# Performance work log

Hardware: AMD Instinct MI355X
Metric: run time of the kernel (lower is better)

The kernel has to match this reference:

```python
import jax, jax.numpy as jnp
import numpy as np

N_GAUSS, H, W, SH_DEG = 1024, 256, 256, 3

SH_C0 = 0.28209479177387814
SH_C1 = 0.4886025119029199
SH_C2 = (1.0925484305920792, -1.0925484305920792, 0.31539156525252005,
         -1.0925484305920792, 0.5462742152960396)
SH_C3 = (-0.5900435899266435, 2.890611442640554, -0.4570457994644658,
         0.3731763325901154, -0.4570457994644658, 1.445305721320277,
         -0.5900435899266435)


def eval_sh(shs, dirs):
    # shs: [N,16,3], dirs: [N,3] normalized. Matches computeColorFromSH (deg 3).
    x, y, z = dirs[:, 0:1], dirs[:, 1:2], dirs[:, 2:3]
    res = SH_C0 * shs[:, 0]
    res = res - SH_C1 * y * shs[:, 1] + SH_C1 * z * shs[:, 2] - SH_C1 * x * shs[:, 3]
    xx, yy, zz = x * x, y * y, z * z
    xy, yz, xz = x * y, y * z, x * z
    res = (res + SH_C2[0] * xy * shs[:, 4] + SH_C2[1] * yz * shs[:, 5]
           + SH_C2[2] * (2.0 * zz - xx - yy) * shs[:, 6]
           + SH_C2[3] * xz * shs[:, 7] + SH_C2[4] * (xx - yy) * shs[:, 8])
    res = (res + SH_C3[0] * y * (3.0 * xx - yy) * shs[:, 9]
           + SH_C3[1] * xy * z * shs[:, 10]
           + SH_C3[2] * y * (4.0 * zz - xx - yy) * shs[:, 11]
           + SH_C3[3] * z * (2.0 * zz - 3.0 * xx - 3.0 * yy) * shs[:, 12]
           + SH_C3[4] * x * (4.0 * zz - xx - yy) * shs[:, 13]
           + SH_C3[5] * z * (xx - yy) * shs[:, 14]
           + SH_C3[6] * x * (xx - yy - zz) * shs[:, 15])
    return jnp.maximum(res + 0.5, 0.0)


def render(background, means3D, opacities, scales, rotations, shs,
           view_mat, proj_mat, cam_pos, tan_fovx, tan_fovy, height, width):
    N = means3D.shape[0]
    tanx, tany = tan_fovx[0], tan_fovy[0]
    fx = width / (2.0 * tanx)
    fy = height / (2.0 * tany)

    # --- 3D covariance: Sigma = R diag(s^2) R^T (computeCov3D) ---
    q = rotations / jnp.linalg.norm(rotations, axis=-1, keepdims=True)
    r, x, y, z = q[:, 0], q[:, 1], q[:, 2], q[:, 3]
    R = jnp.stack([
        jnp.stack([1 - 2 * (y * y + z * z), 2 * (x * y - r * z), 2 * (x * z + r * y)], -1),
        jnp.stack([2 * (x * y + r * z), 1 - 2 * (x * x + z * z), 2 * (y * z - r * x)], -1),
        jnp.stack([2 * (x * z - r * y), 2 * (y * z + r * x), 1 - 2 * (x * x + y * y)], -1),
    ], -2)  # [N,3,3]
    M = R * scales[:, None, :]
    Sigma = jnp.einsum('nij,nkj->nik', M, M)  # [N,3,3]

    # --- view transform + EWA 2D covariance (computeCov2D) ---
    t = means3D @ view_mat[:3, :3].T + view_mat[:3, 3]  # [N,3] camera space
    tz = t[:, 2]
    valid_z = tz > 0.2
    tzs = jnp.where(valid_z, tz, 1.0)
    limx, limy = 1.3 * tanx, 1.3 * tany
    tx = jnp.clip(t[:, 0] / tzs, -limx, limx) * tzs
    ty = jnp.clip(t[:, 1] / tzs, -limy, limy) * tzs
    zeros = jnp.zeros_like(tzs)
    J = jnp.stack([
        jnp.stack([fx / tzs, zeros, -fx * tx / (tzs * tzs)], -1),
        jnp.stack([zeros, fy / tzs, -fy * ty / (tzs * tzs)], -1),
    ], -2)  # [N,2,3]
    T2 = jnp.einsum('nij,jk->nik', J, view_mat[:3, :3])
    cov2d = jnp.einsum('nij,njk,nlk->nil', T2, Sigma, T2)  # [N,2,2]
    a = cov2d[:, 0, 0] + 0.3
    c = cov2d[:, 1, 1] + 0.3
    b = cov2d[:, 0, 1]
    det = a * c - b * b
    valid = valid_z & (det > 0)
    inv_det = jnp.where(det > 0, 1.0 / jnp.where(det > 0, det, 1.0), 0.0)
    conic = jnp.stack([c, -b, a], -1) * inv_det[:, None]  # [N,3]

    # --- projection to pixel coords (ndc2Pix) ---
    ph = jnp.concatenate([means3D, jnp.ones((N, 1), means3D.dtype)], -1) @ proj_mat.T
    p_w = 1.0 / (ph[:, 3] + 1e-7)
    px = ((ph[:, 0] * p_w + 1.0) * width - 1.0) * 0.5
    py = ((ph[:, 1] * p_w + 1.0) * height - 1.0) * 0.5

    # --- SH -> RGB ---
    dirs = means3D - cam_pos[None, :]
    dirs = dirs / jnp.linalg.norm(dirs, axis=-1, keepdims=True)
    colors = eval_sh(shs, dirs)  # [N,3]

    # --- global depth sort (front to back) ---
    depth = jnp.where(valid, tz, 1e10)
    order = jnp.argsort(depth)
    px_s, py_s = px[order], py[order]
    conic_s = conic[order]
    opac_s = opacities[order, 0]
    colors_s = colors[order]
    valid_s = valid[order]

    # --- per-pixel alpha and front-to-back compositing (renderCUDA) ---
    ys, xs = jnp.meshgrid(jnp.arange(height, dtype=jnp.float32),
                          jnp.arange(width, dtype=jnp.float32), indexing='ij')
    pixx, pixy = xs.reshape(-1), ys.reshape(-1)  # [P]
    dx = px_s[:, None] - pixx[None, :]  # [N,P]
    dy = py_s[:, None] - pixy[None, :]
    power = (-0.5 * (conic_s[:, 0:1] * dx * dx + conic_s[:, 2:3] * dy * dy)
             - conic_s[:, 1:2] * dx * dy)
    alpha = jnp.minimum(opac_s[:, None] * jnp.exp(jnp.minimum(power, 0.0)), 0.99)
    keep = (power <= 0.0) & (alpha >= 1.0 / 255.0) & valid_s[:, None]
    alpha = jnp.where(keep, alpha, 0.0)

    Tcum = jnp.cumprod(1.0 - alpha, axis=0)  # [N,P]
    T_prev = jnp.concatenate([jnp.ones((1, alpha.shape[1]), alpha.dtype), Tcum[:-1]], 0)
    wgt = alpha * T_prev
    img = jnp.einsum('nc,np->cp', colors_s, wgt) + background[:, None] * Tcum[-1][None, :]
    return img.reshape(3, height, width)


def setup_inputs() -> dict:
    key = jax.random.key(0)
    ks = jax.random.split(key, 6)
    means3D = jax.random.uniform(ks[0], (N_GAUSS, 3), minval=-3.0, maxval=3.0)
    means3D = means3D.at[:, 2].set(
        jax.random.uniform(ks[1], (N_GAUSS,), minval=2.0, maxval=10.0))
    opacities = jax.random.uniform(ks[2], (N_GAUSS, 1), minval=0.3, maxval=0.95)
    scales = jax.random.uniform(ks[3], (N_GAUSS, 3), minval=0.02, maxval=0.15)
    rotations = jax.random.normal(ks[4], (N_GAUSS, 4))
    shs = jax.random.normal(ks[5], (N_GAUSS, (SH_DEG + 1) ** 2, 3)) * 0.3
    background = jnp.zeros((3,), jnp.float32)
    view_mat = jnp.eye(4, dtype=jnp.float32)  # camera at origin looking +z
    tanx = tany = 0.5
    zn, zf = 0.01, 100.0
    proj = np.zeros((4, 4), np.float32)
    proj[0, 0] = 1.0 / tanx
    proj[1, 1] = 1.0 / tany
    proj[2, 2] = zf / (zf - zn)
    proj[2, 3] = -(zf * zn) / (zf - zn)
    proj[3, 2] = 1.0
    proj_mat = jnp.asarray(proj) @ view_mat  # full projection
    cam_pos = jnp.zeros((3,), jnp.float32)
    return dict(background=background, means3D=means3D, opacities=opacities,
                scales=scales, rotations=rotations, shs=shs, view_mat=view_mat,
                proj_mat=proj_mat, cam_pos=cam_pos,
                tan_fovx=jnp.array([tanx], jnp.float32),
                tan_fovy=jnp.array([tany], jnp.float32), height=H, width=W)


def reference(background, means3D, opacities, scales, rotations, shs,
              view_mat, proj_mat, cam_pos, tan_fovx, tan_fovy, height, width):
    return render(background, means3D, opacities, scales, rotations, shs,
                  view_mat, proj_mat, cam_pos, tan_fovx, tan_fovy, height, width)
```

## Files before the change

### kernel.cpp

```cpp
#include <hip/hip_runtime.h>
#include <math.h>

#define NG 1024
#define LOG2E 1.4426950408889634f


__global__ void prep_kernel(
    const float* __restrict__ means3D, const float* __restrict__ opacities,
    const float* __restrict__ scales,  const float* __restrict__ rotations,
    const float* __restrict__ shs,     const float* __restrict__ view_mat,
    const float* __restrict__ proj_mat,const float* __restrict__ cam_pos,
    const float* __restrict__ tanx_p,  const float* __restrict__ tany_p,
    const int* __restrict__ h_p,       const int* __restrict__ w_p,
    uint4* __restrict__ grec, float4* __restrict__ rec, int N)
{
    int i = blockIdx.x * blockDim.x + threadIdx.x;
    if (i >= N) return;
    float tanx = tanx_p[0], tany = tany_p[0];
    float Wf = (float)w_p[0], Hf = (float)h_p[0];
    int tilesX = w_p[0] >> 3, tilesY = h_p[0] >> 3;
    float fx = Wf / (2.f * tanx), fy = Hf / (2.f * tany);

    float mx = means3D[3*i], my = means3D[3*i+1], mz = means3D[3*i+2];

    float4 q4 = ((const float4*)rotations)[i];
    float qr = q4.x, qx = q4.y, qy = q4.z, qz = q4.w;
    float qn = sqrtf(qr*qr + qx*qx + qy*qy + qz*qz);
    qr /= qn; qx /= qn; qy /= qn; qz /= qn;
    float sx = scales[3*i], sy = scales[3*i+1], sz = scales[3*i+2];
    float R00 = 1.f-2.f*(qy*qy+qz*qz), R01 = 2.f*(qx*qy-qr*qz), R02 = 2.f*(qx*qz+qr*qy);
    float R10 = 2.f*(qx*qy+qr*qz), R11 = 1.f-2.f*(qx*qx+qz*qz), R12 = 2.f*(qy*qz-qr*qx);
    float R20 = 2.f*(qx*qz-qr*qy), R21 = 2.f*(qy*qz+qr*qx), R22 = 1.f-2.f*(qx*qx+qy*qy);
    float M00=R00*sx, M01=R01*sy, M02=R02*sz;
    float M10=R10*sx, M11=R11*sy, M12=R12*sz;
    float M20=R20*sx, M21=R21*sy, M22=R22*sz;
    float S00 = M00*M00+M01*M01+M02*M02;
    float S01 = M00*M10+M01*M11+M02*M12;
    float S02 = M00*M20+M01*M21+M02*M22;
    float S11 = M10*M10+M11*M11+M12*M12;
    float S12 = M10*M20+M11*M21+M12*M22;
    float S22 = M20*M20+M21*M21+M22*M22;

    const float* V = view_mat;
    float t0 = V[0]*mx + V[1]*my + V[2]*mz  + V[3];
    float t1 = V[4]*mx + V[5]*my + V[6]*mz  + V[7];
    float t2 = V[8]*mx + V[9]*my + V[10]*mz + V[11];
    bool valid_z = t2 > 0.2f;
    float tzs = valid_z ? t2 : 1.0f;
    float limx = 1.3f*tanx, limy = 1.3f*tany;
    float txc = fminf(fmaxf(t0/tzs, -limx), limx) * tzs;
    float tyc = fminf(fmaxf(t1/tzs, -limy), limy) * tzs;
    float inv_tz = 1.f / tzs;
    float J00 = fx*inv_tz, J02 = -fx*txc*inv_tz*inv_tz;
    float J11 = fy*inv_tz, J12 = -fy*tyc*inv_tz*inv_tz;
    float T200 = J00*V[0] + J02*V[8];
    float T201 = J00*V[1] + J02*V[9];
    float T202 = J00*V[2] + J02*V[10];
    float T210 = J11*V[4] + J12*V[8];
    float T211 = J11*V[5] + J12*V[9];
    float T212 = J11*V[6] + J12*V[10];
    float u0 = S00*T200 + S01*T201 + S02*T202;
    float u1 = S01*T200 + S11*T201 + S12*T202;
    float u2 = S02*T200 + S12*T201 + S22*T202;
    float cov00 = T200*u0 + T201*u1 + T202*u2;
    float cov01 = T210*u0 + T211*u1 + T212*u2;
    float v0 = S00*T210 + S01*T211 + S02*T212;
    float v1 = S01*T210 + S11*T211 + S12*T212;
    float v2 = S02*T210 + S12*T211 + S22*T212;
    float cov11 = T210*v0 + T211*v1 + T212*v2;
    float a = cov00 + 0.3f;
    float c = cov11 + 0.3f;
    float b = cov01;
    float det = a*c - b*b;
    bool valid = valid_z && (det > 0.f);
    float inv_det = (det > 0.f) ? (1.f/det) : 0.f;
    float Aq = c*inv_det, Bq = -b*inv_det, Cq = a*inv_det;

    const float* P = proj_mat;
    float ph0 = P[0]*mx  + P[1]*my  + P[2]*mz  + P[3];
    float ph1 = P[4]*mx  + P[5]*my  + P[6]*mz  + P[7];
    float ph3 = P[12]*mx + P[13]*my + P[14]*mz + P[15];
    float pw = 1.f / (ph3 + 1e-7f);
    float px = ((ph0*pw + 1.f)*Wf - 1.f)*0.5f;
    float py = ((ph1*pw + 1.f)*Hf - 1.f)*0.5f;

    float dxm = mx - cam_pos[0], dym = my - cam_pos[1], dzm = mz - cam_pos[2];
    float dn = sqrtf(dxm*dxm + dym*dym + dzm*dzm);
    float X = dxm/dn, Y = dym/dn, Z = dzm/dn;
    float xx = X*X, yy = Y*Y, zz = Z*Z;
    float xy = X*Y, yz = Y*Z, xz = X*Z;
    float sc[48];
    {
        const float4* s4 = (const float4*)(shs + i*48);
        #pragma unroll
        for (int k = 0; k < 12; k++) {
            float4 v = s4[k];
            sc[4*k] = v.x; sc[4*k+1] = v.y; sc[4*k+2] = v.z; sc[4*k+3] = v.w;
        }
    }
    float col[3];
    #pragma unroll
    for (int ch = 0; ch < 3; ch++) {
        float res = 0.28209479177387814f * sc[ch];
        res += -0.4886025119029199f * Y * sc[3+ch]
             +  0.4886025119029199f * Z * sc[6+ch]
             -  0.4886025119029199f * X * sc[9+ch];
        res +=  1.0925484305920792f * xy * sc[12+ch]
             + (-1.0925484305920792f) * yz * sc[15+ch]
             +  0.31539156525252005f * (2.f*zz - xx - yy) * sc[18+ch]
             + (-1.0925484305920792f) * xz * sc[21+ch]
             +  0.5462742152960396f * (xx - yy) * sc[24+ch];
        res += -0.5900435899266435f * Y * (3.f*xx - yy) * sc[27+ch]
             +  2.890611442640554f  * xy * Z * sc[30+ch]
             + (-0.4570457994644658f) * Y * (4.f*zz - xx - yy) * sc[33+ch]
             +  0.3731763325901154f  * Z * (2.f*zz - 3.f*xx - 3.f*yy) * sc[36+ch]
             + (-0.4570457994644658f) * X * (4.f*zz - xx - yy) * sc[39+ch]
             +  1.445305721320277f   * Z * (xx - yy) * sc[42+ch]
             + (-0.5900435899266435f) * X * (xx - yy - zz) * sc[45+ch];
        col[ch] = fmaxf(res + 0.5f, 0.f);
    }

    float op = valid ? opacities[i] : 0.f;
    float dpt = valid ? t2 : 1e10f;

    float tau = 2.f * logf(255.f * fmaxf(op, 1e-20f));
    bool has = valid && (op * 255.f > 1.f) && (tau > 0.f);
    float rx = has ? (sqrtf(tau * a) + 0.01f) : 0.f;
    float ry = has ? (sqrtf(tau * c) + 0.01f) : 0.f;

    unsigned trange = 255u;
    if (has) {
        int tx0 = (int)ceilf((px - rx - 7.f) * 0.125f);
        int tx1 = (int)floorf((px + rx) * 0.125f);
        int ty0 = (int)ceilf((py - ry - 7.f) * 0.125f);
        int ty1 = (int)floorf((py + ry) * 0.125f);
        tx0 = max(tx0, 0); ty0 = max(ty0, 0);
        tx1 = min(tx1, tilesX - 1); ty1 = min(ty1, tilesY - 1);
        if (tx0 <= tx1 && ty0 <= ty1)
            trange = (unsigned)tx0 | ((unsigned)tx1 << 8)
                   | ((unsigned)ty0 << 16) | ((unsigned)ty1 << 24);
    }
    grec[i] = make_uint4(__float_as_uint(dpt), (unsigned)i, trange, 0u);

    rec[i*3 + 0] = make_float4(px, py, -0.5f*LOG2E*Aq, -LOG2E*Bq);
    rec[i*3 + 1] = make_float4(-0.5f*LOG2E*Cq, op, col[0], col[1]);
    rec[i*3 + 2] = make_float4(col[2], 0.f, 0.f, 0.f);
}

__device__ inline unsigned long long bstage_shfl(unsigned long long key,
                                                 int tid, int j, int k) {
    unsigned long long partner = __shfl_xor(key, j, 64);
    bool lower = (tid & j) == 0;
    bool asc   = (tid & k) == 0;
    return ((key < partner) == (lower == asc)) ? key : partner;
}

__device__ inline float rlane(float v, int l) {
    return __int_as_float(__builtin_amdgcn_readlane(__float_as_int(v), l));
}

__global__ void __launch_bounds__(64) render_kernel(
    const uint4* __restrict__ grec,
    const float4* __restrict__ rec,
    const float* __restrict__ background,
    float* __restrict__ out,
    int N, int W, int HW)
{
    __shared__ unsigned long long skey[NG];
    int tile = blockIdx.x;
    int tilesX = W >> 3;
    int tx = tile % tilesX, ty = tile / tilesX;
    int lane = threadIdx.x;
    int lx = lane & 7, ly = lane >> 3;
    float pixx = (float)(tx*8 + lx);
    float pixy = (float)(ty*8 + ly);

    int cnt = 0;
    const uint4 miss = make_uint4(0u, 0u, 255u, 0u);
    for (int base = 0; base < N; base += 256) {
        int g0 = base + lane;
        uint4 ra = (g0       < N) ? grec[g0]       : miss;
        uint4 rb = (g0 + 64  < N) ? grec[g0 + 64]  : miss;
        uint4 rc = (g0 + 128 < N) ? grec[g0 + 128] : miss;
        uint4 rd = (g0 + 192 < N) ? grec[g0 + 192] : miss;
        #pragma unroll
        for (int s = 0; s < 4; s++) {
            uint4 r = (s == 0) ? ra : (s == 1) ? rb : (s == 2) ? rc : rd;
            unsigned tr = r.z;
            bool hit = (tx >= (int)(tr & 255u)) & (tx <= (int)((tr >> 8) & 255u))
                     & (ty >= (int)((tr >> 16) & 255u)) & (ty <= (int)(tr >> 24));
            unsigned long long mask = __ballot(hit);
            if (hit) {
                int pos = cnt + __popcll(mask & ((1ull << lane) - 1ull));
                skey[pos] = ((unsigned long long)r.x << 32) | r.y;
            }
            cnt += __popcll(mask);
        }
    }
    __syncthreads();

    float T = 1.f, Cr = 0.f, Cg = 0.f, Cb = 0.f;
    if (cnt > 0 && cnt <= 64) {
        unsigned long long key = (lane < cnt) ? skey[lane] : ~0ull;
        for (int k = 2; k <= 64; k <<= 1)
            for (int j = k >> 1; j >= 1; j >>= 1)
                key = bstage_shfl(key, lane, j, k);
        int gg = (lane < cnt) ? (int)(unsigned)key : 0;
        float4 r0 = rec[gg*3 + 0];
        float4 r1 = rec[gg*3 + 1];
        float4 r2 = rec[gg*3 + 2];
        for (int m = 0; m < cnt; m++) {
            float gpx = rlane(r0.x, m), gpy = rlane(r0.y, m);
            float gA  = rlane(r0.z, m), gB  = rlane(r0.w, m);
            float gC  = rlane(r1.x, m), gop = rlane(r1.y, m);
            float gcr = rlane(r1.z, m), gcg = rlane(r1.w, m);
            float gcb = rlane(r2.x, m);
            float dx = gpx - pixx, dy = gpy - pixy;
            float p2 = fmaf(gA, dx*dx, fmaf(gC, dy*dy, gB*(dx*dy)));
            float e  = __builtin_amdgcn_exp2f(p2);
            float alpha = fminf(gop * e, 0.99f);
            float a2 = (alpha >= (1.f/255.f)) ? alpha : 0.f;
            float w = a2 * T;
            Cr = fmaf(gcr, w, Cr);
            Cg = fmaf(gcg, w, Cg);
            Cb = fmaf(gcb, w, Cb);
            T  = T - a2 * T;
            if ((m & 15) == 15 && __all(T < 1e-4f)) break;
        }
    } else if (cnt > 64) {
        int P = 128;
        while (P < cnt) P <<= 1;
        for (int i2 = cnt + lane; i2 < P; i2 += 64) skey[i2] = ~0ull;
        __syncthreads();
        for (int k = 2; k <= P; k <<= 1) {
            for (int j = k >> 1; j >= 1; j >>= 1) {
                for (int i2 = lane; i2 < P; i2 += 64) {
                    int ixj = i2 ^ j;
                    if (ixj > i2) {
                        bool asc = (i2 & k) == 0;
                        unsigned long long u = skey[i2], v = skey[ixj];
                        if ((u > v) == asc) { skey[i2] = v; skey[ixj] = u; }
                    }
                }
                __syncthreads();
            }
        }
        bool dead = false;
        for (int c = 0; c < cnt && !dead; c += 64) {
            int len = min(64, cnt - c);
            int idx = c + lane;
            int gg = (idx < cnt) ? (int)(unsigned)skey[idx] : 0;
            float4 r0 = rec[gg*3 + 0];
            float4 r1 = rec[gg*3 + 1];
            float4 r2 = rec[gg*3 + 2];
            for (int m = 0; m < len; m++) {
                float gpx = rlane(r0.x, m), gpy = rlane(r0.y, m);
                float gA  = rlane(r0.z, m), gB  = rlane(r0.w, m);
                float gC  = rlane(r1.x, m), gop = rlane(r1.y, m);
                float gcr = rlane(r1.z, m), gcg = rlane(r1.w, m);
                float gcb = rlane(r2.x, m);
                float dx = gpx - pixx, dy = gpy - pixy;
                float p2 = fmaf(gA, dx*dx, fmaf(gC, dy*dy, gB*(dx*dy)));
                float e  = __builtin_amdgcn_exp2f(p2);
                float alpha = fminf(gop * e, 0.99f);
                float a2 = (alpha >= (1.f/255.f)) ? alpha : 0.f;
                float w = a2 * T;
                Cr = fmaf(gcr, w, Cr);
                Cg = fmaf(gcg, w, Cg);
                Cb = fmaf(gcb, w, Cb);
                T  = T - a2 * T;
                if ((m & 15) == 15 && __all(T < 1e-4f)) { dead = true; break; }
            }
            if (__all(T < 1e-4f)) dead = true;
        }
    }

    int p = (ty*8 + ly) * W + tx*8 + lx;
    out[p]        = Cr + background[0]*T;
    out[HW + p]   = Cg + background[1]*T;
    out[2*HW + p] = Cb + background[2]*T;
}

extern "C" void kernel_launch(void* const* d_in, const int* in_sizes, int n_in,
                              void* d_out, int out_size, void* d_ws, size_t ws_size,
                              hipStream_t stream) {
    const float* background = (const float*)d_in[0];
    const float* means3D    = (const float*)d_in[1];
    const float* opacities  = (const float*)d_in[2];
    const float* scales     = (const float*)d_in[3];
    const float* rotations  = (const float*)d_in[4];
    const float* shs        = (const float*)d_in[5];
    const float* view_mat   = (const float*)d_in[6];
    const float* proj_mat   = (const float*)d_in[7];
    const float* cam_pos    = (const float*)d_in[8];
    const float* tanx       = (const float*)d_in[9];
    const float* tany       = (const float*)d_in[10];
    const int*   hp         = (const int*)d_in[11];
    const int*   wp         = (const int*)d_in[12];

    int N  = in_sizes[2];
    int HW = out_size / 3;
    int W  = 256;
    int H  = HW / W;
    float* out = (float*)d_out;

    uint4*  grec = (uint4*)d_ws;
    float4* rec  = (float4*)(grec + NG);

    prep_kernel<<<16, 64, 0, stream>>>(
        means3D, opacities, scales, rotations, shs, view_mat, proj_mat,
        cam_pos, tanx, tany, hp, wp, grec, rec, N);

    int tiles = (W >> 3) * (H >> 3);
    render_kernel<<<tiles, 64, 0, stream>>>(
        grec, rec, background, out, N, W, HW);
}
```

Baseline: 21.78 us.

## Fuse preprocessing and render kernels into one cooperative launch with grid sync

Merges the per-Gaussian preprocessing kernel and the per-tile render kernel into a single cooperative kernel. The first 16 blocks do the preprocessing, then a grid-wide barrier runs before every block renders its tile. This removes one kernel launch and the gap between launches. In exchange it adds a grid sync over 1024 blocks, and the cooperative launch requires the whole grid to be resident at once and may carry extra launch overhead.

```diff
diff --git a/kernel.cpp b/kernel.cpp
--- a/kernel.cpp
+++ b/kernel.cpp
@@ -1,151 +1,12 @@
 #include <hip/hip_runtime.h>
+#include <hip/hip_cooperative_groups.h>
 #include <math.h>
+
+namespace cg = cooperative_groups;
 
 #define NG 1024
 #define LOG2E 1.4426950408889634f
 
-
-__global__ void prep_kernel(
-    const float* __restrict__ means3D, const float* __restrict__ opacities,
-    const float* __restrict__ scales,  const float* __restrict__ rotations,
-    const float* __restrict__ shs,     const float* __restrict__ view_mat,
-    const float* __restrict__ proj_mat,const float* __restrict__ cam_pos,
-    const float* __restrict__ tanx_p,  const float* __restrict__ tany_p,
-    const int* __restrict__ h_p,       const int* __restrict__ w_p,
-    uint4* __restrict__ grec, float4* __restrict__ rec, int N)
-{
-    int i = blockIdx.x * blockDim.x + threadIdx.x;
-    if (i >= N) return;
-    float tanx = tanx_p[0], tany = tany_p[0];
-    float Wf = (float)w_p[0], Hf = (float)h_p[0];
-    int tilesX = w_p[0] >> 3, tilesY = h_p[0] >> 3;
-    float fx = Wf / (2.f * tanx), fy = Hf / (2.f * tany);
-
-    float mx = means3D[3*i], my = means3D[3*i+1], mz = means3D[3*i+2];
-
-    float4 q4 = ((const float4*)rotations)[i];
-    float qr = q4.x, qx = q4.y, qy = q4.z, qz = q4.w;
-    float qn = sqrtf(qr*qr + qx*qx + qy*qy + qz*qz);
-    qr /= qn; qx /= qn; qy /= qn; qz /= qn;
-    float sx = scales[3*i], sy = scales[3*i+1], sz = scales[3*i+2];
-    float R00 = 1.f-2.f*(qy*qy+qz*qz), R01 = 2.f*(qx*qy-qr*qz), R02 = 2.f*(qx*qz+qr*qy);
-    float R10 = 2.f*(qx*qy+qr*qz), R11 = 1.f-2.f*(qx*qx+qz*qz), R12 = 2.f*(qy*qz-qr*qx);
-    float R20 = 2.f*(qx*qz-qr*qy), R21 = 2.f*(qy*qz+qr*qx), R22 = 1.f-2.f*(qx*qx+qy*qy);
-    float M00=R00*sx, M01=R01*sy, M02=R02*sz;
-    float M10=R10*sx, M11=R11*sy, M12=R12*sz;
-    float M20=R20*sx, M21=R21*sy, M22=R22*sz;
-    float S00 = M00*M00+M01*M01+M02*M02;
-    float S01 = M00*M10+M01*M11+M02*M12;
-    float S02 = M00*M20+M01*M21+M02*M22;
-    float S11 = M10*M10+M11*M11+M12*M12;
-    float S12 = M10*M20+M11*M21+M12*M22;
-    float S22 = M20*M20+M21*M21+M22*M22;
-
-    const float* V = view_mat;
-    float t0 = V[0]*mx + V[1]*my + V[2]*mz  + V[3];
-    float t1 = V[4]*mx + V[5]*my + V[6]*mz  + V[7];
-    float t2 = V[8]*mx + V[9]*my + V[10]*mz + V[11];
-    bool valid_z = t2 > 0.2f;
-    float tzs = valid_z ? t2 : 1.0f;
-    float limx = 1.3f*tanx, limy = 1.3f*tany;
-    float txc = fminf(fmaxf(t0/tzs, -limx), limx) * tzs;
-    float tyc = fminf(fmaxf(t1/tzs, -limy), limy) * tzs;
-    float inv_tz = 1.f / tzs;
-    float J00 = fx*inv_tz, J02 = -fx*txc*inv_tz*inv_tz;
-    float J11 = fy*inv_tz, J12 = -fy*tyc*inv_tz*inv_tz;
-    float T200 = J00*V[0] + J02*V[8];
-    float T201 = J00*V[1] + J02*V[9];
-    float T202 = J00*V[2] + J02*V[10];
-    float T210 = J11*V[4] + J12*V[8];
-    float T211 = J11*V[5] + J12*V[9];
-    float T212 = J11*V[6] + J12*V[10];
-    float u0 = S00*T200 + S01*T201 + S02*T202;
-    float u1 = S01*T200 + S11*T201 + S12*T202;
-    float u2 = S02*T200 + S12*T201 + S22*T202;
-    float cov00 = T200*u0 + T201*u1 + T202*u2;
-    float cov01 = T210*u0 + T211*u1 + T212*u2;
-    float v0 = S00*T210 + S01*T211 + S02*T212;
-    float v1 = S01*T210 + S11*T211 + S12*T212;
-    float v2 = S02*T210 + S12*T211 + S22*T212;
-    float cov11 = T210*v0 + T211*v1 + T212*v2;
-    float a = cov00 + 0.3f;
-    float c = cov11 + 0.3f;
-    float b = cov01;
-    float det = a*c - b*b;
-    bool valid = valid_z && (det > 0.f);
-    float inv_det = (det > 0.f) ? (1.f/det) : 0.f;
-    float Aq = c*inv_det, Bq = -b*inv_det, Cq = a*inv_det;
-
-    const float* P = proj_mat;
-    float ph0 = P[0]*mx  + P[1]*my  + P[2]*mz  + P[3];
-    float ph1 = P[4]*mx  + P[5]*my  + P[6]*mz  + P[7];
-    float ph3 = P[12]*mx + P[13]*my + P[14]*mz + P[15];
-    float pw = 1.f / (ph3 + 1e-7f);
-    float px = ((ph0*pw + 1.f)*Wf - 1.f)*0.5f;
-    float py = ((ph1*pw + 1.f)*Hf - 1.f)*0.5f;
-
-    float dxm = mx - cam_pos[0], dym = my - cam_pos[1], dzm = mz - cam_pos[2];
-    float dn = sqrtf(dxm*dxm + dym*dym + dzm*dzm);
-    float X = dxm/dn, Y = dym/dn, Z = dzm/dn;
-    float xx = X*X, yy = Y*Y, zz = Z*Z;
-    float xy = X*Y, yz = Y*Z, xz = X*Z;
-    float sc[48];
-    {
-        const float4* s4 = (const float4*)(shs + i*48);
-        #pragma unroll
-        for (int k = 0; k < 12; k++) {
-            float4 v = s4[k];
-            sc[4*k] = v.x; sc[4*k+1] = v.y; sc[4*k+2] = v.z; sc[4*k+3] = v.w;
-        }
-    }
-    float col[3];
-    #pragma unroll
-    for (int ch = 0; ch < 3; ch++) {
-        float res = 0.28209479177387814f * sc[ch];
-        res += -0.4886025119029199f * Y * sc[3+ch]
-             +  0.4886025119029199f * Z * sc[6+ch]
-             -  0.4886025119029199f * X * sc[9+ch];
-        res +=  1.0925484305920792f * xy * sc[12+ch]
-             + (-1.0925484305920792f) * yz * sc[15+ch]
-             +  0.31539156525252005f * (2.f*zz - xx - yy) * sc[18+ch]
-             + (-1.0925484305920792f) * xz * sc[21+ch]
-             +  0.5462742152960396f * (xx - yy) * sc[24+ch];
-        res += -0.5900435899266435f * Y * (3.f*xx - yy) * sc[27+ch]
-             +  2.890611442640554f  * xy * Z * sc[30+ch]
-             + (-0.4570457994644658f) * Y * (4.f*zz - xx - yy) * sc[33+ch]
-             +  0.3731763325901154f  * Z * (2.f*zz - 3.f*xx - 3.f*yy) * sc[36+ch]
-             + (-0.4570457994644658f) * X * (4.f*zz - xx - yy) * sc[39+ch]
-             +  1.445305721320277f   * Z * (xx - yy) * sc[42+ch]
-             + (-0.5900435899266435f) * X * (xx - yy - zz) * sc[45+ch];
-        col[ch] = fmaxf(res + 0.5f, 0.f);
-    }
-
-    float op = valid ? opacities[i] : 0.f;
-    float dpt = valid ? t2 : 1e10f;
-
-    float tau = 2.f * logf(255.f * fmaxf(op, 1e-20f));
-    bool has = valid && (op * 255.f > 1.f) && (tau > 0.f);
-    float rx = has ? (sqrtf(tau * a) + 0.01f) : 0.f;
-    float ry = has ? (sqrtf(tau * c) + 0.01f) : 0.f;
-
-    unsigned trange = 255u;
-    if (has) {
-        int tx0 = (int)ceilf((px - rx - 7.f) * 0.125f);
-        int tx1 = (int)floorf((px + rx) * 0.125f);
-        int ty0 = (int)ceilf((py - ry - 7.f) * 0.125f);
-        int ty1 = (int)floorf((py + ry) * 0.125f);
-        tx0 = max(tx0, 0); ty0 = max(ty0, 0);
-        tx1 = min(tx1, tilesX - 1); ty1 = min(ty1, tilesY - 1);
-        if (tx0 <= tx1 && ty0 <= ty1)
-            trange = (unsigned)tx0 | ((unsigned)tx1 << 8)
-                   | ((unsigned)ty0 << 16) | ((unsigned)ty1 << 24);
-    }
-    grec[i] = make_uint4(__float_as_uint(dpt), (unsigned)i, trange, 0u);
-
-    rec[i*3 + 0] = make_float4(px, py, -0.5f*LOG2E*Aq, -LOG2E*Bq);
-    rec[i*3 + 1] = make_float4(-0.5f*LOG2E*Cq, op, col[0], col[1]);
-    rec[i*3 + 2] = make_float4(col[2], 0.f, 0.f, 0.f);
-}
 
 __device__ inline unsigned long long bstage_shfl(unsigned long long key,
                                                  int tid, int j, int k) {
@@ -159,18 +20,158 @@
     return __int_as_float(__builtin_amdgcn_readlane(__float_as_int(v), l));
 }
 
-__global__ void __launch_bounds__(64) render_kernel(
-    const uint4* __restrict__ grec,
-    const float4* __restrict__ rec,
-    const float* __restrict__ background,
-    float* __restrict__ out,
+__global__ void __launch_bounds__(64) fused_kernel(
+    const float* __restrict__ means3D, const float* __restrict__ opacities,
+    const float* __restrict__ scales,  const float* __restrict__ rotations,
+    const float* __restrict__ shs,     const float* __restrict__ view_mat,
+    const float* __restrict__ proj_mat,const float* __restrict__ cam_pos,
+    const float* __restrict__ tanx_p,  const float* __restrict__ tany_p,
+    const int* __restrict__ h_p,       const int* __restrict__ w_p,
+    uint4* __restrict__ grec, float4* __restrict__ rec,
+    const float* __restrict__ background, float* __restrict__ out,
     int N, int W, int HW)
 {
     __shared__ unsigned long long skey[NG];
-    int tile = blockIdx.x;
+    int blk  = blockIdx.x;
+    int lane = threadIdx.x;
+
+    int i = blk * 64 + lane;
+    if (blk < (N + 63) / 64 && i < N) {
+        float tanx = tanx_p[0], tany = tany_p[0];
+        float Wf = (float)w_p[0], Hf = (float)h_p[0];
+        int tilesX = w_p[0] >> 3, tilesY = h_p[0] >> 3;
+        float fx = Wf / (2.f * tanx), fy = Hf / (2.f * tany);
+
+        float mx = means3D[3*i], my = means3D[3*i+1], mz = means3D[3*i+2];
+
+        float4 q4 = ((const float4*)rotations)[i];
+        float qr = q4.x, qx = q4.y, qy = q4.z, qz = q4.w;
+        float qn = sqrtf(qr*qr + qx*qx + qy*qy + qz*qz);
+        qr /= qn; qx /= qn; qy /= qn; qz /= qn;
+        float sx = scales[3*i], sy = scales[3*i+1], sz = scales[3*i+2];
+        float R00 = 1.f-2.f*(qy*qy+qz*qz), R01 = 2.f*(qx*qy-qr*qz), R02 = 2.f*(qx*qz+qr*qy);
+        float R10 = 2.f*(qx*qy+qr*qz), R11 = 1.f-2.f*(qx*qx+qz*qz), R12 = 2.f*(qy*qz-qr*qx);
+        float R20 = 2.f*(qx*qz-qr*qy), R21 = 2.f*(qy*qz+qr*qx), R22 = 1.f-2.f*(qx*qx+qy*qy);
+        float M00=R00*sx, M01=R01*sy, M02=R02*sz;
+        float M10=R10*sx, M11=R11*sy, M12=R12*sz;
+        float M20=R20*sx, M21=R21*sy, M22=R22*sz;
+        float S00 = M00*M00+M01*M01+M02*M02;
+        float S01 = M00*M10+M01*M11+M02*M12;
+        float S02 = M00*M20+M01*M21+M02*M22;
+        float S11 = M10*M10+M11*M11+M12*M12;
+        float S12 = M10*M20+M11*M21+M12*M22;
+        float S22 = M20*M20+M21*M21+M22*M22;
+
+        const float* V = view_mat;
+        float t0 = V[0]*mx + V[1]*my + V[2]*mz  + V[3];
+        float t1 = V[4]*mx + V[5]*my + V[6]*mz  + V[7];
+        float t2 = V[8]*mx + V[9]*my + V[10]*mz + V[11];
+        bool valid_z = t2 > 0.2f;
+        float tzs = valid_z ? t2 : 1.0f;
+        float limx = 1.3f*tanx, limy = 1.3f*tany;
+        float txc = fminf(fmaxf(t0/tzs, -limx), limx) * tzs;
+        float tyc = fminf(fmaxf(t1/tzs, -limy), limy) * tzs;
+        float inv_tz = 1.f / tzs;
+        float J00 = fx*inv_tz, J02 = -fx*txc*inv_tz*inv_tz;
+        float J11 = fy*inv_tz, J12 = -fy*tyc*inv_tz*inv_tz;
+        float T200 = J00*V[0] + J02*V[8];
+        float T201 = J00*V[1] + J02*V[9];
+        float T202 = J00*V[2] + J02*V[10];
+        float T210 = J11*V[4] + J12*V[8];
+        float T211 = J11*V[5] + J12*V[9];
+        float T212 = J11*V[6] + J12*V[10];
+        float u0 = S00*T200 + S01*T201 + S02*T202;
+        float u1 = S01*T200 + S11*T201 + S12*T202;
+        float u2 = S02*T200 + S12*T201 + S22*T202;
+        float cov00 = T200*u0 + T201*u1 + T202*u2;
+        float cov01 = T210*u0 + T211*u1 + T212*u2;
+        float v0 = S00*T210 + S01*T211 + S02*T212;
+        float v1 = S01*T210 + S11*T211 + S12*T212;
+        float v2 = S02*T210 + S12*T211 + S22*T212;
+        float cov11 = T210*v0 + T211*v1 + T212*v2;
+        float a = cov00 + 0.3f;
+        float c = cov11 + 0.3f;
+        float b = cov01;
+        float det = a*c - b*b;
+        bool valid = valid_z && (det > 0.f);
+        float inv_det = (det > 0.f) ? (1.f/det) : 0.f;
+        float Aq = c*inv_det, Bq = -b*inv_det, Cq = a*inv_det;
+
+        const float* P = proj_mat;
+        float ph0 = P[0]*mx  + P[1]*my  + P[2]*mz  + P[3];
+        float ph1 = P[4]*mx  + P[5]*my  + P[6]*mz  + P[7];
+        float ph3 = P[12]*mx + P[13]*my + P[14]*mz + P[15];
+        float pw = 1.f / (ph3 + 1e-7f);
+        float px = ((ph0*pw + 1.f)*Wf - 1.f)*0.5f;
+        float py = ((ph1*pw + 1.f)*Hf - 1.f)*0.5f;
+
+        float dxm = mx - cam_pos[0], dym = my - cam_pos[1], dzm = mz - cam_pos[2];
+        float dn = sqrtf(dxm*dxm + dym*dym + dzm*dzm);
+        float X = dxm/dn, Y = dym/dn, Z = dzm/dn;
+        float xx = X*X, yy = Y*Y, zz = Z*Z;
+        float xy = X*Y, yz = Y*Z, xz = X*Z;
+        float sc[48];
+        {
+            const float4* s4 = (const float4*)(shs + i*48);
+            #pragma unroll
+            for (int k = 0; k < 12; k++) {
+                float4 v = s4[k];
+                sc[4*k] = v.x; sc[4*k+1] = v.y; sc[4*k+2] = v.z; sc[4*k+3] = v.w;
+            }
+        }
+        float col[3];
+        #pragma unroll
+        for (int ch = 0; ch < 3; ch++) {
+            float res = 0.28209479177387814f * sc[ch];
+            res += -0.4886025119029199f * Y * sc[3+ch]
+                 +  0.4886025119029199f * Z * sc[6+ch]
+                 -  0.4886025119029199f * X * sc[9+ch];
+            res +=  1.0925484305920792f * xy * sc[12+ch]
+                 + (-1.0925484305920792f) * yz * sc[15+ch]
+                 +  0.31539156525252005f * (2.f*zz - xx - yy) * sc[18+ch]
+                 + (-1.0925484305920792f) * xz * sc[21+ch]
+                 +  0.5462742152960396f * (xx - yy) * sc[24+ch];
+            res += -0.5900435899266435f * Y * (3.f*xx - yy) * sc[27+ch]
+                 +  2.890611442640554f  * xy * Z * sc[30+ch]
+                 + (-0.4570457994644658f) * Y * (4.f*zz - xx - yy) * sc[33+ch]
+                 +  0.3731763325901154f  * Z * (2.f*zz - 3.f*xx - 3.f*yy) * sc[36+ch]
+                 + (-0.4570457994644658f) * X * (4.f*zz - xx - yy) * sc[39+ch]
+                 +  1.445305721320277f   * Z * (xx - yy) * sc[42+ch]
+                 + (-0.5900435899266435f) * X * (xx - yy - zz) * sc[45+ch];
+            col[ch] = fmaxf(res + 0.5f, 0.f);
+        }
+
+        float op = valid ? opacities[i] : 0.f;
+        float dpt = valid ? t2 : 1e10f;
+
+        float tau = 2.f * logf(255.f * fmaxf(op, 1e-20f));
+        bool has = valid && (op * 255.f > 1.f) && (tau > 0.f);
+        float rx = has ? (sqrtf(tau * a) + 0.01f) : 0.f;
+        float ry = has ? (sqrtf(tau * c) + 0.01f) : 0.f;
+
+        unsigned trange = 255u;
+        if (has) {
+            int tx0 = (int)ceilf((px - rx - 7.f) * 0.125f);
+            int tx1 = (int)floorf((px + rx) * 0.125f);
+            int ty0 = (int)ceilf((py - ry - 7.f) * 0.125f);
+            int ty1 = (int)floorf((py + ry) * 0.125f);
+            tx0 = max(tx0, 0); ty0 = max(ty0, 0);
+            tx1 = min(tx1, tilesX - 1); ty1 = min(ty1, tilesY - 1);
+            if (tx0 <= tx1 && ty0 <= ty1)
+                trange = (unsigned)tx0 | ((unsigned)tx1 << 8)
+                       | ((unsigned)ty0 << 16) | ((unsigned)ty1 << 24);
+        }
+        grec[i] = make_uint4(__float_as_uint(dpt), (unsigned)i, trange, 0u);
+
+        rec[i*3 + 0] = make_float4(px, py, -0.5f*LOG2E*Aq, -LOG2E*Bq);
+        rec[i*3 + 1] = make_float4(-0.5f*LOG2E*Cq, op, col[0], col[1]);
+        rec[i*3 + 2] = make_float4(col[2], 0.f, 0.f, 0.f);
+    }
+
+    cg::this_grid().sync();
+
     int tilesX = W >> 3;
-    int tx = tile % tilesX, ty = tile / tilesX;
-    int lane = threadIdx.x;
+    int tx = blk % tilesX, ty = blk / tilesX;
     int lx = lane & 7, ly = lane >> 3;
     float pixx = (float)(tx*8 + lx);
     float pixy = (float)(ty*8 + ly);
@@ -307,11 +308,15 @@
     uint4*  grec = (uint4*)d_ws;
     float4* rec  = (float4*)(grec + NG);
 
-    prep_kernel<<<16, 64, 0, stream>>>(
-        means3D, opacities, scales, rotations, shs, view_mat, proj_mat,
-        cam_pos, tanx, tany, hp, wp, grec, rec, N);
-
     int tiles = (W >> 3) * (H >> 3);
-    render_kernel<<<tiles, 64, 0, stream>>>(
-        grec, rec, background, out, N, W, HW);
+
+    void* args[] = {
+        (void*)&means3D, (void*)&opacities, (void*)&scales, (void*)&rotations,
+        (void*)&shs, (void*)&view_mat, (void*)&proj_mat, (void*)&cam_pos,
+        (void*)&tanx, (void*)&tany, (void*)&hp, (void*)&wp,
+        (void*)&grec, (void*)&rec, (void*)&background, (void*)&out,
+        (void*)&N, (void*)&W, (void*)&HW
+    };
+    hipLaunchCooperativeKernel((void*)fused_kernel, dim3(tiles), dim3(64),
+                               args, 0, stream);
 }
```

After: 79.85 us. +266.6%, slower.
